# Optimization experiments

Measured on AMD Instinct MI355X. Metric: run time of the kernel, lower is better.

Reference implementation:

```python
import jax, jax.numpy as jnp
import numpy as np

VOCAB, EBD, ATT_H, R, T, IMG_C = 50257, 512, 512, 196, 1024, 512


def setup_inputs() -> dict:
    key = jax.random.key(0)
    ks = jax.random.split(key, 10)
    question = jax.random.randint(ks[0], (T,), 0, VOCAB)
    img_feat = jax.random.normal(ks[1], (R, IMG_C), dtype=jnp.float32)
    emb_table = (jax.random.normal(ks[2], (VOCAB, EBD), dtype=jnp.float32) * 0.02).at[0].set(0.0)  # padding_idx=0
    W_img = jax.random.normal(ks[3], (EBD, IMG_C), dtype=jnp.float32) * (1.0 / np.sqrt(IMG_C))
    b_img = jnp.zeros((EBD,), dtype=jnp.float32)
    W_ai = jax.random.normal(ks[4], (ATT_H, EBD), dtype=jnp.float32) * (1.0 / np.sqrt(EBD))  # att_img, no bias
    W_aw = jax.random.normal(ks[5], (ATT_H, EBD), dtype=jnp.float32) * (1.0 / np.sqrt(EBD))  # att_word
    b_aw = jnp.zeros((ATT_H,), dtype=jnp.float32)
    w_att = jax.random.normal(ks[6], (ATT_H,), dtype=jnp.float32) * (1.0 / np.sqrt(ATT_H))  # att -> scalar
    b_att = jnp.zeros((), dtype=jnp.float32)
    return {"question": question, "img_feat": img_feat, "emb_table": emb_table,
            "W_img": W_img, "b_img": b_img, "W_ai": W_ai, "W_aw": W_aw,
            "b_aw": b_aw, "w_att": w_att, "b_att": b_att}


def reference(question, img_feat, emb_table, W_img, b_img, W_ai, W_aw, b_aw, w_att, b_att):
    # img_feature = relu(Linear(512 -> ebd)(vgg_regions));  [R, EBD]
    img = jax.nn.relu(img_feat @ W_img.T + b_img)
    # per-word embeddings  [T, EBD]
    E = emb_table[question]
    # additive attention: tanh(attImg[r] + attWord[t]) . w_att + b_att  -> [T, R]
    AI = img @ W_ai.T                       # [R, H]
    AW = E @ W_aw.T + b_aw                  # [T, H]
    scores = jnp.einsum('trh,h->tr', jnp.tanh(AI[None, :, :] + AW[:, None, :]), w_att) + b_att
    w = jax.nn.softmax(scores, axis=-1)     # softmax over regions, [T, R]
    # weighted sum of img features, divided by n_regions (faithful to original)
    ctx = (w @ img) / img.shape[0]          # [T, EBD]
    # attedInput: concat(new_img_feature, word_emd)  [T, 2*EBD]
    return jnp.concatenate([ctx, E], axis=-1)
```

## Files before the change

kernel.cpp:

```cpp
#include <hip/hip_runtime.h>

#define PRESCALE 2.8853900817779268f

typedef short s16;
typedef unsigned short u16;
typedef unsigned int u32;
typedef __attribute__((ext_vector_type(8))) short short8v;
typedef __attribute__((ext_vector_type(4))) float f4;

#if __has_builtin(__builtin_amdgcn_exp2f)
#define EXP2(x) __builtin_amdgcn_exp2f(x)
#else
static __device__ inline float exp2_raw(float x){ float r; asm("v_exp_f32 %0, %1":"=v"(r):"v"(x)); return r; }
#define EXP2(x) exp2_raw(x)
#endif
#if __has_builtin(__builtin_amdgcn_rcpf)
#define RCP(x) __builtin_amdgcn_rcpf(x)
#else
static __device__ inline float rcp_raw(float x){ float r; asm("v_rcp_f32 %0, %1":"=v"(r):"v"(x)); return r; }
#define RCP(x) rcp_raw(x)
#endif

__device__ inline u16 f2bf(float f){
  union{u32 i; float f;} v; v.f = f;
  u32 r = v.i + 0x7fffu + ((v.i >> 16) & 1u);
  return (u16)(r >> 16);
}

__global__ __launch_bounds__(256) void k_prep(
    const float* __restrict__ W_img, const float* __restrict__ W_ai,
    const float* __restrict__ W_aw,  const float* __restrict__ img_feat,
    const int* __restrict__ question, const float* __restrict__ emb,
    s16* __restrict__ Wb, s16* __restrict__ Xb, s16* __restrict__ Eb,
    float* __restrict__ out){
  for (int g = blockIdx.x*256 + threadIdx.x; g < 360448; g += gridDim.x*256){
    if (g < 196608){
      const int i = g*4, w = i >> 18;
      const float sc = (w == 0) ? 1.f : PRESCALE;
      const float* src = (w==0) ? W_img : ((w==1) ? W_ai : W_aw);
      float4 v = *reinterpret_cast<const float4*>(src + (i & 262143));
      ushort4 o; o.x=f2bf(v.x*sc); o.y=f2bf(v.y*sc); o.z=f2bf(v.z*sc); o.w=f2bf(v.w*sc);
      *reinterpret_cast<ushort4*>(Wb + i) = o;
    } else if (g < 229376){
      const int i = (g - 196608)*4;
      ushort4 o = make_ushort4(0,0,0,0);
      if ((i >> 9) < 196){
        float4 v = *reinterpret_cast<const float4*>(img_feat + i);
        o.x=f2bf(v.x); o.y=f2bf(v.y); o.z=f2bf(v.z); o.w=f2bf(v.w);
      }
      *reinterpret_cast<ushort4*>(Xb + i) = o;
    } else {
      const int i = (g - 229376)*4;
      const int t = i >> 9, c = i & 511;
      float4 v = *reinterpret_cast<const float4*>(emb + (size_t)question[t]*512 + c);
      *reinterpret_cast<float4*>(out + (size_t)t*1024 + 512 + c) = v;
      ushort4 o; o.x=f2bf(v.x); o.y=f2bf(v.y); o.z=f2bf(v.z); o.w=f2bf(v.w);
      *reinterpret_cast<ushort4*>(Eb + i) = o;
    }
  }
}

__device__ inline void mfma_core(const s16* __restrict__ A, const s16* __restrict__ B,
                                 int m0, int n0, int lr, int lg, f4 acc[2][2]){
  const s16* pa0 = A + (size_t)(m0 + lr)*512 + lg*8;
  const s16* pa1 = pa0 + 16*512;
  const s16* pb0 = B + (size_t)(n0 + lr)*512 + lg*8;
  const s16* pb1 = pb0 + 16*512;
  #pragma unroll 4
  for (int k = 0; k < 512; k += 32){
    short8v a0 = *reinterpret_cast<const short8v*>(pa0 + k);
    short8v a1 = *reinterpret_cast<const short8v*>(pa1 + k);
    short8v b0 = *reinterpret_cast<const short8v*>(pb0 + k);
    short8v b1 = *reinterpret_cast<const short8v*>(pb1 + k);
    acc[0][0] = __builtin_amdgcn_mfma_f32_16x16x32_bf16(a0, b0, acc[0][0], 0, 0, 0);
    acc[0][1] = __builtin_amdgcn_mfma_f32_16x16x32_bf16(a0, b1, acc[0][1], 0, 0, 0);
    acc[1][0] = __builtin_amdgcn_mfma_f32_16x16x32_bf16(a1, b0, acc[1][0], 0, 0, 0);
    acc[1][1] = __builtin_amdgcn_mfma_f32_16x16x32_bf16(a1, b1, acc[1][1], 0, 0, 0);
  }
}

__global__ __launch_bounds__(256) void k_gemms(
    const s16* __restrict__ Xb, const s16* __restrict__ Wb_img,
    const s16* __restrict__ Wb_aw, const s16* __restrict__ Eb,
    const float* __restrict__ b_img, const float* __restrict__ b_aw,
    float* __restrict__ img, s16* __restrict__ img_b,
    float* __restrict__ AWT4){
  const int tid = threadIdx.x, w = tid>>6, l = tid&63;
  const int lr = l & 15, lg = l >> 4;
  f4 acc[2][2] = {};
  if (blockIdx.x < 32){
    const int m0 = (blockIdx.x >> 3)*64 + (w>>1)*32;
    const int n0 = (blockIdx.x & 7)*64 + (w&1)*32;
    mfma_core(Xb, Wb_img, m0, n0, lr, lg, acc);
    #pragma unroll
    for (int i = 0; i < 2; ++i){
      #pragma unroll
      for (int j = 0; j < 2; ++j){
        const int nn = n0 + j*16 + lr;
        const float bc = b_img[nn];
        #pragma unroll
        for (int p = 0; p < 4; ++p){
          const int mm = m0 + i*16 + lg*4 + p;
          float v = fmaxf(acc[i][j][p] + bc, 0.f);
          img[(size_t)mm*512 + nn] = v;
          img_b[(size_t)mm*512 + nn] = (s16)f2bf(v);
        }
      }
    }
  } else {
    const int blk = blockIdx.x - 32;
    const int m0 = (blk >> 4)*64 + (w>>1)*32;
    const int n0 = (blk & 15)*64 + (w&1)*32;
    mfma_core(Wb_aw, Eb, m0, n0, lr, lg, acc);
    #pragma unroll
    for (int i = 0; i < 2; ++i){
      const int mb = m0 + i*16 + lg*4;
      #pragma unroll
      for (int j = 0; j < 2; ++j){
        const int nn = n0 + j*16 + lr;
        f4 o;
        #pragma unroll
        for (int p = 0; p < 4; ++p)
          o[p] = acc[i][j][p] + b_aw[mb+p]*PRESCALE;
        *reinterpret_cast<f4*>(AWT4 + (size_t)(mb>>2)*4096 + nn*4) = o;
      }
    }
  }
}

__global__ __launch_bounds__(256) void k_ai(
    const s16* __restrict__ img_b, const s16* __restrict__ Wb_ai,
    float* __restrict__ AI){
  const int tid = threadIdx.x, w = tid>>6, l = tid&63;
  const int lr = l & 15, lg = l >> 4;
  const int m0 = (blockIdx.x >> 3)*64 + (w>>1)*32;
  const int n0 = (blockIdx.x & 7)*64 + (w&1)*32;
  f4 acc[2][2] = {};
  mfma_core(img_b, Wb_ai, m0, n0, lr, lg, acc);
  #pragma unroll
  for (int i = 0; i < 2; ++i)
    #pragma unroll
    for (int j = 0; j < 2; ++j){
      const int nn = n0 + j*16 + lr;
      #pragma unroll
      for (int p = 0; p < 4; ++p){
        const int mm = m0 + i*16 + lg*4 + p;
        AI[(size_t)mm*512 + nn] = acc[i][j][p];
      }
    }
}

#define RB5 5
__global__ __launch_bounds__(512) void k_score(
    const float* __restrict__ AI, const float* __restrict__ AWT4,
    const float* __restrict__ w_att, float* __restrict__ STp){
  __shared__ float ais[RB5][64];
  __shared__ float wsh[64];
  const int tid = threadIdx.x, w = tid>>6, l = tid&63;
  const int rr = blockIdx.x, hc = blockIdx.y, th = blockIdx.z;
  const int r0 = rr*RB5, h0 = hc*64;
  if (tid < 80){
    const int i = tid >> 4, j = tid & 15;
    const int r = min(r0 + i, 195);
    *reinterpret_cast<f4*>(&ais[i][j*4]) =
        *reinterpret_cast<const f4*>(AI + (size_t)r*512 + h0 + j*4);
  } else if (tid < 96){
    const int j = tid - 80;
    *reinterpret_cast<f4*>(&wsh[j*4]) =
        *reinterpret_cast<const f4*>(w_att + h0 + j*4);
  }
  const int t = th*512 + w*64 + l;
  const int hg0 = hc*16;
  f4 awr[16];
  #pragma unroll
  for (int j = 0; j < 16; ++j)
    awr[j] = *reinterpret_cast<const f4*>(AWT4 + (size_t)(hg0+j)*4096 + t*4);
  __syncthreads();
  #pragma unroll
  for (int i = 0; i < RB5; ++i){
    const int r = r0 + i;
    if (r >= 196) break;
    float a0=0.f, a1=0.f, a2=0.f, a3=0.f;
    #pragma unroll
    for (int j = 0; j < 16; ++j){
      f4 av = *reinterpret_cast<const f4*>(&ais[i][j*4]);
      f4 wv = *reinterpret_cast<const f4*>(&wsh[j*4]);
      a0 += wv.x*RCP(EXP2(av.x+awr[j].x)+1.f);
      a1 += wv.y*RCP(EXP2(av.y+awr[j].y)+1.f);
      a2 += wv.z*RCP(EXP2(av.z+awr[j].z)+1.f);
      a3 += wv.w*RCP(EXP2(av.w+awr[j].w)+1.f);
    }
    STp[((size_t)hc<<18) + (size_t)r*1024 + t] = (a0+a1)+(a2+a3);
  }
}

__global__ __launch_bounds__(256) void k_ctx(
    const float* __restrict__ STp, const float* __restrict__ img,
    float* __restrict__ out){
  __shared__ float wgt[196][16];
  __shared__ float red[16][16];
  const int tid = threadIdx.x;
  const int t0 = blockIdx.x*16, e0 = blockIdx.y*64;
  const int rs = tid>>4, tl = tid&15;

  float m = 1e30f;
  for (int k = 0; k < 13; ++k){
    const int r = rs + 16*k;
    if (r < 196){
      float s = 0.f;
      #pragma unroll
      for (int c = 0; c < 8; ++c)
        s += STp[((size_t)c<<18) + (size_t)r*1024 + t0 + tl];
      wgt[r][tl] = s;
      m = fminf(m, s);
    }
  }
  red[rs][tl] = m;
  __syncthreads();
  if (tid < 16){
    float mm = red[0][tid];
    #pragma unroll
    for (int i = 1; i < 16; ++i) mm = fminf(mm, red[i][tid]);
    red[0][tid] = mm;
  }
  __syncthreads();
  const float mt = red[0][tl];
  float sum = 0.f;
  for (int k = 0; k < 13; ++k){
    const int r = rs + 16*k;
    if (r < 196){
      float p = EXP2(PRESCALE*(mt - wgt[r][tl]));
      wgt[r][tl] = p;
      sum += p;
    }
  }
  __syncthreads();
  red[rs][tl] = sum;
  __syncthreads();
  if (tid < 16){
    float ss = 0.f;
    #pragma unroll
    for (int i = 0; i < 16; ++i) ss += red[i][tid];
    red[0][tid] = 1.f / (ss * 196.f);
  }
  __syncthreads();
  const float inv = red[0][tl];
  for (int k = 0; k < 13; ++k){
    const int r = rs + 16*k;
    if (r < 196) wgt[r][tl] *= inv;
  }
  __syncthreads();

  const int e = e0 + (tid & 63), tq = tid >> 6;
  float acc[4] = {0.f, 0.f, 0.f, 0.f};
  const float* ip = img + e;
  #pragma unroll 4
  for (int r = 0; r < 196; ++r){
    const float f = ip[(size_t)r*512];
    float4 w4 = *reinterpret_cast<const float4*>(&wgt[r][tq*4]);
    acc[0] += w4.x*f; acc[1] += w4.y*f; acc[2] += w4.z*f; acc[3] += w4.w*f;
  }
  #pragma unroll
  for (int j = 0; j < 4; ++j)
    out[(size_t)(t0 + tq*4 + j)*1024 + e] = acc[j];
}

extern "C" void kernel_launch(void* const* d_in, const int* in_sizes, int n_in,
                              void* d_out, int out_size, void* d_ws, size_t ws_size,
                              hipStream_t stream) {
  const int*   question = (const int*)d_in[0];
  const float* img_feat = (const float*)d_in[1];
  const float* emb      = (const float*)d_in[2];
  const float* W_img    = (const float*)d_in[3];
  const float* b_img    = (const float*)d_in[4];
  const float* W_ai     = (const float*)d_in[5];
  const float* W_aw     = (const float*)d_in[6];
  const float* b_aw     = (const float*)d_in[7];
  const float* w_att    = (const float*)d_in[8];
  float* out = (float*)d_out;

  char* ws = (char*)d_ws;
  s16*   Wb    = (s16*)(ws);
  s16*   Xb    = (s16*)(ws + 1572864);
  s16*   Eb    = (s16*)(ws + 1835008);
  float* img   = (float*)(ws + 2883584);
  s16*   img_b = (s16*)(ws + 3407872);
  float* AI    = (float*)(ws + 3670016);
  float* AWT4  = (float*)(ws + 4194304);
  float* STp   = (float*)(ws + 6291456);

  hipLaunchKernelGGL(k_prep,  dim3(512),    dim3(256), 0, stream,
                     W_img, W_ai, W_aw, img_feat, question, emb, Wb, Xb, Eb, out);
  hipLaunchKernelGGL(k_gemms, dim3(160),    dim3(256), 0, stream,
                     Xb, Wb, Wb + 2*262144, Eb, b_img, b_aw, img, img_b, AWT4);
  hipLaunchKernelGGL(k_ai,    dim3(32),     dim3(256), 0, stream,
                     img_b, Wb + 262144, AI);
  hipLaunchKernelGGL(k_score, dim3(40,8,2), dim3(512), 0, stream,
                     AI, AWT4, w_att, STp);
  hipLaunchKernelGGL(k_ctx,   dim3(64,8),   dim3(256), 0, stream, STp, img, out);
}
```

Before: 79.88 us.

## Fuse image attention projection GEMM into score kernel

Drops the separate k_ai launch and the global AI buffer. Each k_score block now computes its own AI tile (region rows by 64 hidden units) with bf16 MFMA straight into shared memory before the tanh-score loop. Region blocking changes from 5 to 8 rows with a 26-block x grid, and the bounds check is removed; rows past 196 read padded workspace and are written to unused score slots. This saves a kernel launch and a global write/read round trip. In exchange, every z-slice recomputes the GEMM tile and half of each 16-row MFMA tile is discarded.

After: 79.39 us. About the same (-0.6%).

```diff
diff --git a/kernel.cpp b/kernel.cpp
--- a/kernel.cpp
+++ b/kernel.cpp
@@ -128,58 +128,45 @@
   }
 }
 
-__global__ __launch_bounds__(256) void k_ai(
+__global__ __launch_bounds__(512) void k_score(
     const s16* __restrict__ img_b, const s16* __restrict__ Wb_ai,
-    float* __restrict__ AI){
+    const float* __restrict__ AWT4, const float* __restrict__ w_att,
+    float* __restrict__ STp){
+  __shared__ float ais[16][68];
+  __shared__ float wsh[64];
   const int tid = threadIdx.x, w = tid>>6, l = tid&63;
   const int lr = l & 15, lg = l >> 4;
-  const int m0 = (blockIdx.x >> 3)*64 + (w>>1)*32;
-  const int n0 = (blockIdx.x & 7)*64 + (w&1)*32;
-  f4 acc[2][2] = {};
-  mfma_core(img_b, Wb_ai, m0, n0, lr, lg, acc);
-  #pragma unroll
-  for (int i = 0; i < 2; ++i)
-    #pragma unroll
-    for (int j = 0; j < 2; ++j){
-      const int nn = n0 + j*16 + lr;
-      #pragma unroll
-      for (int p = 0; p < 4; ++p){
-        const int mm = m0 + i*16 + lg*4 + p;
-        AI[(size_t)mm*512 + nn] = acc[i][j][p];
-      }
-    }
-}
-
-#define RB5 5
-__global__ __launch_bounds__(512) void k_score(
-    const float* __restrict__ AI, const float* __restrict__ AWT4,
-    const float* __restrict__ w_att, float* __restrict__ STp){
-  __shared__ float ais[RB5][64];
-  __shared__ float wsh[64];
-  const int tid = threadIdx.x, w = tid>>6, l = tid&63;
-  const int rr = blockIdx.x, hc = blockIdx.y, th = blockIdx.z;
-  const int r0 = rr*RB5, h0 = hc*64;
-  if (tid < 80){
-    const int i = tid >> 4, j = tid & 15;
-    const int r = min(r0 + i, 195);
-    *reinterpret_cast<f4*>(&ais[i][j*4]) =
-        *reinterpret_cast<const f4*>(AI + (size_t)r*512 + h0 + j*4);
-  } else if (tid < 96){
-    const int j = tid - 80;
-    *reinterpret_cast<f4*>(&wsh[j*4]) =
-        *reinterpret_cast<const f4*>(w_att + h0 + j*4);
-  }
-  const int t = th*512 + w*64 + l;
-  const int hg0 = hc*16;
+  const int r0 = blockIdx.x*8, h0 = blockIdx.y*64;
+
+  if (w < 4){
+    const s16* pa = img_b + (size_t)(r0 + lr)*512 + lg*8;
+    const s16* pb = Wb_ai + (size_t)(h0 + w*16 + lr)*512 + lg*8;
+    f4 acc = {};
+    #pragma unroll 4
+    for (int ks = 0; ks < 16; ++ks){
+      short8v a = *reinterpret_cast<const short8v*>(pa + ks*32);
+      short8v b = *reinterpret_cast<const short8v*>(pb + ks*32);
+      acc = __builtin_amdgcn_mfma_f32_16x16x32_bf16(a, b, acc, 0, 0, 0);
+    }
+    #pragma unroll
+    for (int p = 0; p < 4; ++p)
+      ais[lg*4 + p][w*16 + lr] = acc[p];
+  }
+  if (tid < 16)
+    *reinterpret_cast<f4*>(&wsh[tid*4]) =
+        *reinterpret_cast<const f4*>(w_att + h0 + tid*4);
+  __syncthreads();
+
+  const int t = blockIdx.z*512 + w*64 + l;
+  const int hg0 = blockIdx.y*16;
   f4 awr[16];
   #pragma unroll
   for (int j = 0; j < 16; ++j)
     awr[j] = *reinterpret_cast<const f4*>(AWT4 + (size_t)(hg0+j)*4096 + t*4);
-  __syncthreads();
+
   #pragma unroll
-  for (int i = 0; i < RB5; ++i){
+  for (int i = 0; i < 8; ++i){
     const int r = r0 + i;
-    if (r >= 196) break;
     float a0=0.f, a1=0.f, a2=0.f, a3=0.f;
     #pragma unroll
     for (int j = 0; j < 16; ++j){
@@ -190,7 +177,7 @@
       a2 += wv.z*RCP(EXP2(av.z+awr[j].z)+1.f);
       a3 += wv.w*RCP(EXP2(av.w+awr[j].w)+1.f);
     }
-    STp[((size_t)hc<<18) + (size_t)r*1024 + t] = (a0+a1)+(a2+a3);
+    STp[((size_t)blockIdx.y<<18) + (size_t)r*1024 + t] = (a0+a1)+(a2+a3);
   }
 }
 
@@ -285,7 +272,6 @@
   s16*   Eb    = (s16*)(ws + 1835008);
   float* img   = (float*)(ws + 2883584);
   s16*   img_b = (s16*)(ws + 3407872);
-  float* AI    = (float*)(ws + 3670016);
   float* AWT4  = (float*)(ws + 4194304);
   float* STp   = (float*)(ws + 6291456);
 
@@ -293,9 +279,7 @@
                      W_img, W_ai, W_aw, img_feat, question, emb, Wb, Xb, Eb, out);
   hipLaunchKernelGGL(k_gemms, dim3(160),    dim3(256), 0, stream,
                      Xb, Wb, Wb + 2*262144, Eb, b_img, b_aw, img, img_b, AWT4);
-  hipLaunchKernelGGL(k_ai,    dim3(32),     dim3(256), 0, stream,
-                     img_b, Wb + 262144, AI);
-  hipLaunchKernelGGL(k_score, dim3(40,8,2), dim3(512), 0, stream,
-                     AI, AWT4, w_att, STp);
+  hipLaunchKernelGGL(k_score, dim3(26,8,2), dim3(512), 0, stream,
+                     img_b, Wb + 262144, AWT4, w_att, STp);
   hipLaunchKernelGGL(k_ctx,   dim3(64,8),   dim3(256), 0, stream, STp, img, out);
 }
```

## Fuse bf16 prep, GEMMs and AI projection into one front kernel

Applied to the files above, without the earlier changes.

Replaces the separate prep, GEMM and AI kernels with a single k_front kernel. It converts fp32 operands to bf16 in registers with v_cvt_pk_bf16_f32 instead of writing bf16 copies to workspace. The image-linear result is kept in LDS and fed straight into the AI projection, and the embedding gather is done directly inside the AW GEMM. This removes two launches and the workspace round trips. In exchange, W_img and W_ai are re-read and re-converted by every image block, the image branch runs on only 13 blocks with long serial work each, and the prescale is now applied after accumulation.

New measurement: 150.8 us. +88.7%, slower.

```diff
diff --git a/kernel.cpp b/kernel.cpp
--- a/kernel.cpp
+++ b/kernel.cpp
@@ -26,92 +26,101 @@
   u32 r = v.i + 0x7fffu + ((v.i >> 16) & 1u);
   return (u16)(r >> 16);
 }
-
-__global__ __launch_bounds__(256) void k_prep(
-    const float* __restrict__ W_img, const float* __restrict__ W_ai,
-    const float* __restrict__ W_aw,  const float* __restrict__ img_feat,
-    const int* __restrict__ question, const float* __restrict__ emb,
-    s16* __restrict__ Wb, s16* __restrict__ Xb, s16* __restrict__ Eb,
+__device__ inline u32 cvt2(float lo, float hi){
+  u32 r; asm("v_cvt_pk_bf16_f32 %0, %1, %2" : "=v"(r) : "v"(lo), "v"(hi)); return r;
+}
+__device__ inline short8v cvt8(f4 a, f4 b){
+  union { u32 u[4]; short8v s; } x;
+  x.u[0] = cvt2(a.x, a.y); x.u[1] = cvt2(a.z, a.w);
+  x.u[2] = cvt2(b.x, b.y); x.u[3] = cvt2(b.z, b.w);
+  return x.s;
+}
+__device__ inline f4 ldf4(const float* p){ return *reinterpret_cast<const f4*>(p); }
+
+#define LDSP 520
+__global__ __launch_bounds__(256) void k_front(
+    const int* __restrict__ question, const float* __restrict__ img_feat,
+    const float* __restrict__ emb,
+    const float* __restrict__ W_img, const float* __restrict__ b_img,
+    const float* __restrict__ W_ai,  const float* __restrict__ W_aw,
+    const float* __restrict__ b_aw,
+    float* __restrict__ img, float* __restrict__ AI, float* __restrict__ AWT4,
     float* __restrict__ out){
-  for (int g = blockIdx.x*256 + threadIdx.x; g < 360448; g += gridDim.x*256){
-    if (g < 196608){
-      const int i = g*4, w = i >> 18;
-      const float sc = (w == 0) ? 1.f : PRESCALE;
-      const float* src = (w==0) ? W_img : ((w==1) ? W_ai : W_aw);
-      float4 v = *reinterpret_cast<const float4*>(src + (i & 262143));
-      ushort4 o; o.x=f2bf(v.x*sc); o.y=f2bf(v.y*sc); o.z=f2bf(v.z*sc); o.w=f2bf(v.w*sc);
-      *reinterpret_cast<ushort4*>(Wb + i) = o;
-    } else if (g < 229376){
-      const int i = (g - 196608)*4;
-      ushort4 o = make_ushort4(0,0,0,0);
-      if ((i >> 9) < 196){
-        float4 v = *reinterpret_cast<const float4*>(img_feat + i);
-        o.x=f2bf(v.x); o.y=f2bf(v.y); o.z=f2bf(v.z); o.w=f2bf(v.w);
-      }
-      *reinterpret_cast<ushort4*>(Xb + i) = o;
-    } else {
-      const int i = (g - 229376)*4;
-      const int t = i >> 9, c = i & 511;
-      float4 v = *reinterpret_cast<const float4*>(emb + (size_t)question[t]*512 + c);
-      *reinterpret_cast<float4*>(out + (size_t)t*1024 + 512 + c) = v;
-      ushort4 o; o.x=f2bf(v.x); o.y=f2bf(v.y); o.z=f2bf(v.z); o.w=f2bf(v.w);
-      *reinterpret_cast<ushort4*>(Eb + i) = o;
-    }
-  }
-}
-
-__device__ inline void mfma_core(const s16* __restrict__ A, const s16* __restrict__ B,
-                                 int m0, int n0, int lr, int lg, f4 acc[2][2]){
-  const s16* pa0 = A + (size_t)(m0 + lr)*512 + lg*8;
-  const s16* pa1 = pa0 + 16*512;
-  const s16* pb0 = B + (size_t)(n0 + lr)*512 + lg*8;
-  const s16* pb1 = pb0 + 16*512;
-  #pragma unroll 4
-  for (int k = 0; k < 512; k += 32){
-    short8v a0 = *reinterpret_cast<const short8v*>(pa0 + k);
-    short8v a1 = *reinterpret_cast<const short8v*>(pa1 + k);
-    short8v b0 = *reinterpret_cast<const short8v*>(pb0 + k);
-    short8v b1 = *reinterpret_cast<const short8v*>(pb1 + k);
-    acc[0][0] = __builtin_amdgcn_mfma_f32_16x16x32_bf16(a0, b0, acc[0][0], 0, 0, 0);
-    acc[0][1] = __builtin_amdgcn_mfma_f32_16x16x32_bf16(a0, b1, acc[0][1], 0, 0, 0);
-    acc[1][0] = __builtin_amdgcn_mfma_f32_16x16x32_bf16(a1, b0, acc[1][0], 0, 0, 0);
-    acc[1][1] = __builtin_amdgcn_mfma_f32_16x16x32_bf16(a1, b1, acc[1][1], 0, 0, 0);
-  }
-}
-
-__global__ __launch_bounds__(256) void k_gemms(
-    const s16* __restrict__ Xb, const s16* __restrict__ Wb_img,
-    const s16* __restrict__ Wb_aw, const s16* __restrict__ Eb,
-    const float* __restrict__ b_img, const float* __restrict__ b_aw,
-    float* __restrict__ img, s16* __restrict__ img_b,
-    float* __restrict__ AWT4){
+  __shared__ u16 limg[16*LDSP];
   const int tid = threadIdx.x, w = tid>>6, l = tid&63;
   const int lr = l & 15, lg = l >> 4;
-  f4 acc[2][2] = {};
-  if (blockIdx.x < 32){
-    const int m0 = (blockIdx.x >> 3)*64 + (w>>1)*32;
-    const int n0 = (blockIdx.x & 7)*64 + (w&1)*32;
-    mfma_core(Xb, Wb_img, m0, n0, lr, lg, acc);
-    #pragma unroll
-    for (int i = 0; i < 2; ++i){
-      #pragma unroll
-      for (int j = 0; j < 2; ++j){
-        const int nn = n0 + j*16 + lr;
-        const float bc = b_img[nn];
+
+  if (blockIdx.x < 13){
+    const int r0 = blockIdx.x*16;
+    {
+      const float* pa = img_feat + (size_t)min(r0+lr,195)*512 + lg*8;
+      const float* pb = W_img + (size_t)(w*128 + lr)*512 + lg*8;
+      f4 acc[8] = {};
+      for (int ks = 0; ks < 16; ++ks){
+        short8v av = cvt8(ldf4(pa + ks*32), ldf4(pa + ks*32 + 4));
+        #pragma unroll
+        for (int nf = 0; nf < 8; ++nf){
+          const float* pbn = pb + (size_t)nf*16*512 + ks*32;
+          short8v bv = cvt8(ldf4(pbn), ldf4(pbn + 4));
+          acc[nf] = __builtin_amdgcn_mfma_f32_16x16x32_bf16(av, bv, acc[nf], 0, 0, 0);
+        }
+      }
+      #pragma unroll
+      for (int nf = 0; nf < 8; ++nf){
+        const int e = w*128 + nf*16 + lr;
+        const float bc = b_img[e];
         #pragma unroll
         for (int p = 0; p < 4; ++p){
-          const int mm = m0 + i*16 + lg*4 + p;
-          float v = fmaxf(acc[i][j][p] + bc, 0.f);
-          img[(size_t)mm*512 + nn] = v;
-          img_b[(size_t)mm*512 + nn] = (s16)f2bf(v);
+          const int rr = lg*4 + p;
+          float v = fmaxf(acc[nf][p] + bc, 0.f);
+          img[(size_t)(r0+rr)*512 + e] = v;
+          limg[rr*LDSP + e] = f2bf(v);
         }
       }
     }
-  } else {
-    const int blk = blockIdx.x - 32;
+    __syncthreads();
+    {
+      const u16* la = limg + lr*LDSP + lg*8;
+      const float* pb = W_ai + (size_t)(w*128 + lr)*512 + lg*8;
+      f4 acc[8] = {};
+      for (int ks = 0; ks < 16; ++ks){
+        short8v av = *reinterpret_cast<const short8v*>(la + ks*32);
+        #pragma unroll
+        for (int nf = 0; nf < 8; ++nf){
+          const float* pbn = pb + (size_t)nf*16*512 + ks*32;
+          short8v bv = cvt8(ldf4(pbn), ldf4(pbn + 4));
+          acc[nf] = __builtin_amdgcn_mfma_f32_16x16x32_bf16(av, bv, acc[nf], 0, 0, 0);
+        }
+      }
+      #pragma unroll
+      for (int nf = 0; nf < 8; ++nf){
+        const int h = w*128 + nf*16 + lr;
+        #pragma unroll
+        for (int p = 0; p < 4; ++p)
+          AI[(size_t)(r0 + lg*4 + p)*512 + h] = acc[nf][p] * PRESCALE;
+      }
+    }
+  } else if (blockIdx.x < 141){
+    const int blk = blockIdx.x - 13;
     const int m0 = (blk >> 4)*64 + (w>>1)*32;
     const int n0 = (blk & 15)*64 + (w&1)*32;
-    mfma_core(Wb_aw, Eb, m0, n0, lr, lg, acc);
+    const int q0 = question[n0 + lr], q1 = question[n0 + 16 + lr];
+    const float* pa0 = W_aw + (size_t)(m0 + lr)*512 + lg*8;
+    const float* pa1 = pa0 + (size_t)16*512;
+    const float* pe0 = emb + (size_t)q0*512 + lg*8;
+    const float* pe1 = emb + (size_t)q1*512 + lg*8;
+    f4 acc[2][2] = {};
+    for (int ks = 0; ks < 16; ++ks){
+      const int o = ks*32;
+      short8v a0 = cvt8(ldf4(pa0 + o), ldf4(pa0 + o + 4));
+      short8v a1 = cvt8(ldf4(pa1 + o), ldf4(pa1 + o + 4));
+      short8v b0 = cvt8(ldf4(pe0 + o), ldf4(pe0 + o + 4));
+      short8v b1 = cvt8(ldf4(pe1 + o), ldf4(pe1 + o + 4));
+      acc[0][0] = __builtin_amdgcn_mfma_f32_16x16x32_bf16(a0, b0, acc[0][0], 0, 0, 0);
+      acc[0][1] = __builtin_amdgcn_mfma_f32_16x16x32_bf16(a0, b1, acc[0][1], 0, 0, 0);
+      acc[1][0] = __builtin_amdgcn_mfma_f32_16x16x32_bf16(a1, b0, acc[1][0], 0, 0, 0);
+      acc[1][1] = __builtin_amdgcn_mfma_f32_16x16x32_bf16(a1, b1, acc[1][1], 0, 0, 0);
+    }
     #pragma unroll
     for (int i = 0; i < 2; ++i){
       const int mb = m0 + i*16 + lg*4;
@@ -121,33 +130,19 @@
         f4 o;
         #pragma unroll
         for (int p = 0; p < 4; ++p)
-          o[p] = acc[i][j][p] + b_aw[mb+p]*PRESCALE;
+          o[p] = (acc[i][j][p] + b_aw[mb+p]) * PRESCALE;
         *reinterpret_cast<f4*>(AWT4 + (size_t)(mb>>2)*4096 + nn*4) = o;
       }
     }
-  }
-}
-
-__global__ __launch_bounds__(256) void k_ai(
-    const s16* __restrict__ img_b, const s16* __restrict__ Wb_ai,
-    float* __restrict__ AI){
-  const int tid = threadIdx.x, w = tid>>6, l = tid&63;
-  const int lr = l & 15, lg = l >> 4;
-  const int m0 = (blockIdx.x >> 3)*64 + (w>>1)*32;
-  const int n0 = (blockIdx.x & 7)*64 + (w&1)*32;
-  f4 acc[2][2] = {};
-  mfma_core(img_b, Wb_ai, m0, n0, lr, lg, acc);
-  #pragma unroll
-  for (int i = 0; i < 2; ++i)
-    #pragma unroll
-    for (int j = 0; j < 2; ++j){
-      const int nn = n0 + j*16 + lr;
-      #pragma unroll
-      for (int p = 0; p < 4; ++p){
-        const int mm = m0 + i*16 + lg*4 + p;
-        AI[(size_t)mm*512 + nn] = acc[i][j][p];
-      }
-    }
+  } else {
+    const int t = (blockIdx.x - 141)*16 + (tid >> 4);
+    const int c0 = (tid & 15)*32;
+    const float* er = emb + (size_t)question[t]*512 + c0;
+    float* orow = out + (size_t)t*1024 + 512 + c0;
+    #pragma unroll
+    for (int qd = 0; qd < 8; ++qd)
+      *reinterpret_cast<f4*>(orow + qd*4) = ldf4(er + qd*4);
+  }
 }
 
 #define RB5 5
@@ -280,21 +275,14 @@
   float* out = (float*)d_out;
 
   char* ws = (char*)d_ws;
-  s16*   Wb    = (s16*)(ws);
-  s16*   Xb    = (s16*)(ws + 1572864);
-  s16*   Eb    = (s16*)(ws + 1835008);
-  float* img   = (float*)(ws + 2883584);
-  s16*   img_b = (s16*)(ws + 3407872);
-  float* AI    = (float*)(ws + 3670016);
-  float* AWT4  = (float*)(ws + 4194304);
-  float* STp   = (float*)(ws + 6291456);
-
-  hipLaunchKernelGGL(k_prep,  dim3(512),    dim3(256), 0, stream,
-                     W_img, W_ai, W_aw, img_feat, question, emb, Wb, Xb, Eb, out);
-  hipLaunchKernelGGL(k_gemms, dim3(160),    dim3(256), 0, stream,
-                     Xb, Wb, Wb + 2*262144, Eb, b_img, b_aw, img, img_b, AWT4);
-  hipLaunchKernelGGL(k_ai,    dim3(32),     dim3(256), 0, stream,
-                     img_b, Wb + 262144, AI);
+  float* img   = (float*)(ws);
+  float* AI    = (float*)(ws + 524288);
+  float* AWT4  = (float*)(ws + 1048576);
+  float* STp   = (float*)(ws + 3145728);
+
+  hipLaunchKernelGGL(k_front, dim3(205),    dim3(256), 0, stream,
+                     question, img_feat, emb, W_img, b_img, W_ai, W_aw, b_aw,
+                     img, AI, AWT4, out);
   hipLaunchKernelGGL(k_score, dim3(40,8,2), dim3(512), 0, stream,
                      AI, AWT4, w_att, STp);
   hipLaunchKernelGGL(k_ctx,   dim3(64,8),   dim3(256), 0, stream, STp, img, out);
```
